# Optimization experiments

Measured on AMD Instinct MI355X. Metric: run time of the kernel, lower is better.

The kernel has to match this reference:

```python
import jax, jax.numpy as jnp
import numpy as np

HEADS = 8
DIM_HEAD = 64
WINDOW = 8  # local_window_size


def _sn_weight(W, u, sigma):
    """SNLinear reparameterized weight: one power-iteration step (detached)
    then sigma_W = v^T W u (grad flows through W only), weight = W/sigma_W * sigma."""
    v = W @ u
    v = v / jnp.linalg.norm(v)
    u2 = W.T @ v
    u2 = u2 / jnp.linalg.norm(u2)
    v = jax.lax.stop_gradient(v)
    u2 = jax.lax.stop_gradient(u2)
    sigma_w = jnp.einsum('c,cd,d->', v, W, u2)
    return W / sigma_w * sigma


def setup_inputs() -> dict:
    key = jax.random.key(0)
    ks = jax.random.split(key, 6)
    B, S, D = 2, 2048, 512
    inner = HEADS * DIM_HEAD  # 512
    x = jax.random.normal(ks[0], (B, S, D), dtype=jnp.float32)
    W_qkv = 0.02 * jax.random.normal(ks[1], (3 * inner, D), dtype=jnp.float32)
    u_qkv = jax.random.normal(ks[2], (D,), dtype=jnp.float32)
    u_qkv = u_qkv / jnp.linalg.norm(u_qkv)
    W_out = 0.02 * jax.random.normal(ks[3], (D, inner), dtype=jnp.float32)
    b_out = jnp.zeros((D,), dtype=jnp.float32)
    u_out = jax.random.normal(ks[4], (inner,), dtype=jnp.float32)
    u_out = u_out / jnp.linalg.norm(u_out)
    sigma_qkv = jnp.ones((1,), dtype=jnp.float32)
    sigma_out = jnp.ones((1,), dtype=jnp.float32)
    temperature = jnp.asarray(np.log(DIM_HEAD ** -0.5), dtype=jnp.float32)
    return {
        'x': x, 'W_qkv': W_qkv, 'u_qkv': u_qkv, 'sigma_qkv': sigma_qkv,
        'W_out': W_out, 'b_out': b_out, 'u_out': u_out, 'sigma_out': sigma_out,
        'temperature': temperature,
    }


def reference(x, W_qkv, u_qkv, sigma_qkv, W_out, b_out, u_out, sigma_out, temperature):
    B, S, D = x.shape
    # qkv projection (spectral-normed, no bias)
    Wq = _sn_weight(W_qkv, u_qkv, sigma_qkv[0])
    qkv = x @ Wq.T                                   # [B,S,3*inner]
    q, k, v = jnp.split(qkv, 3, axis=-1)
    to_heads = lambda t: t.reshape(B, S, HEADS, DIM_HEAD).transpose(0, 2, 1, 3)
    q, k, v = to_heads(q), to_heads(k), to_heads(v)   # [B,H,S,Dh]
    dots = jnp.einsum('bhid,bhjd->bhij', q, k) * jnp.exp(temperature)
    # local causal band mask (True inside band); original masked_fill fills True
    i = jnp.arange(S)
    band = (i[:, None] >= i[None, :]) & ((i[:, None] - i[None, :]) <= (WINDOW - 1))
    neg = -jnp.finfo(dots.dtype).max
    dots = jnp.where(band[None, None, :, :], neg, dots)
    attn = jax.nn.softmax(dots, axis=-1)
    out = jnp.einsum('bhij,bhjd->bhid', attn, v)      # [B,H,S,Dh]
    out = out.transpose(0, 2, 1, 3).reshape(B, S, HEADS * DIM_HEAD)
    Wo = _sn_weight(W_out, u_out, sigma_out[0])
    return out @ Wo.T + b_out
```

## Files before the change

### kernel.cpp

```cpp
#include <hip/hip_runtime.h>
#include <hip/hip_bf16.h>
#include <math.h>

#define HEADS 8
#define DH 64
#define SEQ 2048
#define BATCH 2
#define DMODEL 512
#define INNER 512
#define WIN 8

typedef unsigned short ushort_t;
typedef __attribute__((ext_vector_type(8))) __bf16 bf16x8;
typedef __attribute__((ext_vector_type(8))) unsigned short u16x8;
typedef __attribute__((ext_vector_type(4))) float f32x4;

__device__ inline float bf2f(ushort_t u) {
    unsigned v = ((unsigned)u) << 16; float f; __builtin_memcpy(&f, &v, 4); return f;
}
__device__ inline ushort_t f2bf(float f) {
    __hip_bfloat16 h = __float2bfloat16(f); ushort_t u; __builtin_memcpy(&u, &h, 2); return u;
}
__device__ inline int swz_idx(int row, int col) { return ((row << 6) | col) ^ ((row & 7) << 3); }

__device__ inline bf16x8 ld_frag(const ushort_t* lds, int row, int col) {
    u16x8 v = *(const u16x8*)&lds[swz_idx(row, col)];
    return __builtin_bit_cast(bf16x8, v);
}
__device__ inline f32x4 mfma16(bf16x8 a, bf16x8 b, f32x4 c) {
    return __builtin_amdgcn_mfma_f32_16x16x32_bf16(a, b, c, 0, 0, 0);
}
__device__ inline void gload16(const void* g, void* l) {
    __builtin_amdgcn_global_load_lds(
        (const __attribute__((address_space(1))) unsigned int*)g,
        (__attribute__((address_space(3))) unsigned int*)l, 16, 0, 0);
}

__global__ __launch_bounds__(256) void fused_cast_sn1(const float* __restrict__ x,
                                                      const float* __restrict__ Wq,
                                                      const float* __restrict__ Wo,
                                                      const float* __restrict__ uq,
                                                      const float* __restrict__ uo,
                                                      ushort_t* __restrict__ xb,
                                                      ushort_t* __restrict__ wqb,
                                                      ushort_t* __restrict__ wob,
                                                      float* __restrict__ zbuf,
                                                      float* __restrict__ v1,
                                                      float* __restrict__ v2) {
    const int b = blockIdx.x;
    if (b < 1536) {
        const int gid = b * 256 + threadIdx.x;
        const float* src; ushort_t* dst; int g;
        if (gid < 262144)      { src = x;  dst = xb;  g = gid; }
        else if (gid < 360448) { src = Wq; dst = wqb; g = gid - 262144; }
        else                   { src = Wo; dst = wob; g = gid - 360448; }
        float4 a = *(const float4*)&src[(size_t)g * 8];
        float4 c = *(const float4*)&src[(size_t)g * 8 + 4];
        u16x8 o;
        o[0] = f2bf(a.x); o[1] = f2bf(a.y); o[2] = f2bf(a.z); o[3] = f2bf(a.w);
        o[4] = f2bf(c.x); o[5] = f2bf(c.y); o[6] = f2bf(c.z); o[7] = f2bf(c.w);
        *(u16x8*)&dst[(size_t)g * 8] = o;
        if (gid < 1032) zbuf[gid] = 0.f;
    } else {
        const int lane = threadIdx.x & 63, w = threadIdx.x >> 6;
        const int r = (b - 1536) * 4 + w;
        const float* W; const float* u; float* vout; int rr;
        if (r < 1536) { W = Wq; u = uq; vout = v1; rr = r; }
        else          { W = Wo; u = uo; vout = v2; rr = r - 1536; }
        float4 w0 = *(const float4*)&W[(size_t)rr * 512 + lane * 8];
        float4 w1 = *(const float4*)&W[(size_t)rr * 512 + lane * 8 + 4];
        float4 u0 = *(const float4*)&u[lane * 8];
        float4 u1 = *(const float4*)&u[lane * 8 + 4];
        float dot = w0.x * u0.x + w0.y * u0.y + w0.z * u0.z + w0.w * u0.w +
                    w1.x * u1.x + w1.y * u1.y + w1.z * u1.z + w1.w * u1.w;
#pragma unroll
        for (int off = 1; off < 64; off <<= 1) dot += __shfl_xor(dot, off, 64);
        if (lane == 0) vout[rr] = dot;
    }
}

__global__ __launch_bounds__(256) void fused_sn2_sn3(const float* __restrict__ Wq,
                                                     const float* __restrict__ Wo,
                                                     const float* __restrict__ v1,
                                                     const float* __restrict__ v2,
                                                     float* __restrict__ z1,
                                                     float* __restrict__ z2,
                                                     float* __restrict__ counter,
                                                     const float* __restrict__ sq,
                                                     const float* __restrict__ so,
                                                     float* __restrict__ scales) {
    __shared__ float red[256];
    __shared__ int is_last;
    const int t = threadIdx.x, b = blockIdx.x;
    {
        const float* W; const float* v; float* z; int r0;
        if (b < 96) { W = Wq; v = v1; z = z1; r0 = b * 16; }
        else        { W = Wo; v = v2; z = z2; r0 = (b - 96) * 16; }
        float a0 = 0.f, a1 = 0.f;
        for (int i = 0; i < 16; ++i) {
            float vv = v[r0 + i];
            a0 += W[(size_t)(r0 + i) * 512 + t] * vv;
            a1 += W[(size_t)(r0 + i) * 512 + 256 + t] * vv;
        }
        atomicAdd(&z[t], a0);
        atomicAdd(&z[t + 256], a1);
    }
    __threadfence();
    __syncthreads();
    if (t == 0) is_last = (atomicAdd(counter, 1.0f) == 127.0f);
    __syncthreads();
    if (!is_last) return;
    __threadfence();
    for (int which = 0; which < 2; ++which) {
        const float* v = which ? v2 : v1;
        const float* z = which ? z2 : z1;
        const int R = which ? 512 : 1536;
        float n1 = 0.f;
        for (int i = t; i < R; i += 256) { float q = v[i]; n1 += q * q; }
        red[t] = n1; __syncthreads();
        for (int off = 128; off > 0; off >>= 1) { if (t < off) red[t] += red[t + off]; __syncthreads(); }
        n1 = red[0]; __syncthreads();
        float n2 = 0.f;
        for (int i = t; i < 512; i += 256) { float q = z[i]; n2 += q * q; }
        red[t] = n2; __syncthreads();
        for (int off = 128; off > 0; off >>= 1) { if (t < off) red[t] += red[t + off]; __syncthreads(); }
        if (t == 0) scales[which] = (which ? so[0] : sq[0]) * sqrtf(n1 / red[0]);
        __syncthreads();
    }
}

__global__ __launch_bounds__(256) void gemm_bt_qkv(const ushort_t* __restrict__ A,
                                                   const ushort_t* __restrict__ B,
                                                   ushort_t* __restrict__ qkv) {
    constexpr int K = DMODEL;
    __shared__ ushort_t As[8 * 128 * 8];
    __shared__ ushort_t Bs[8 * 128 * 8];
    const int t = threadIdx.x, lane = t & 63, w = t >> 6;
    const int wm = w >> 1, wn = w & 1, lg = lane >> 4, li = lane & 15;
    const int m0 = blockIdx.y * 128, n0 = blockIdx.x * 128;
    f32x4 acc[4][4] = {};
    for (int k0 = 0; k0 < K; k0 += 64) {
        __syncthreads();
#pragma unroll
        for (int i = 0; i < 4; ++i) {
            int j = w * 4 + i;
            int kc = j >> 1, mh = (j & 1) * 64;
            gload16(&A[(size_t)(m0 + mh + lane) * K + k0 + kc * 8], &As[(kc * 128 + mh) * 8]);
            gload16(&B[(size_t)(n0 + mh + lane) * K + k0 + kc * 8], &Bs[(kc * 128 + mh) * 8]);
        }
        __syncthreads();
#pragma unroll
        for (int kw = 0; kw < 2; ++kw) {
            bf16x8 af[4], bf[4];
#pragma unroll
            for (int mi = 0; mi < 4; ++mi)
                af[mi] = *(const bf16x8*)&As[((kw * 4 + lg) * 128 + wm * 64 + mi * 16 + li) * 8];
#pragma unroll
            for (int ni = 0; ni < 4; ++ni)
                bf[ni] = *(const bf16x8*)&Bs[((kw * 4 + lg) * 128 + wn * 64 + ni * 16 + li) * 8];
#pragma unroll
            for (int mi = 0; mi < 4; ++mi)
#pragma unroll
                for (int ni = 0; ni < 4; ++ni)
                    acc[mi][ni] = mfma16(af[mi], bf[ni], acc[mi][ni]);
        }
    }
    ushort_t* vT = qkv + (size_t)2 * BATCH * HEADS * SEQ * DH;
    if (n0 >= 1024) {
#pragma unroll
        for (int mi = 0; mi < 4; ++mi) {
            int base = m0 + wm * 64 + mi * 16 + lg * 4;
            int bb = base >> 11, ss = base & 2047;
#pragma unroll
            for (int ni = 0; ni < 4; ++ni) {
                int n = n0 + wn * 64 + ni * 16 + li;
                int h = (n >> 6) & 7, d0 = n & 63;
                ushort4 o;
                o.x = f2bf(acc[mi][ni][0]); o.y = f2bf(acc[mi][ni][1]);
                o.z = f2bf(acc[mi][ni][2]); o.w = f2bf(acc[mi][ni][3]);
                *(ushort4*)&vT[((size_t)((bb * HEADS + h) * DH) + d0) * SEQ + ss] = o;
            }
        }
    } else {
#pragma unroll
        for (int mi = 0; mi < 4; ++mi)
#pragma unroll
            for (int r = 0; r < 4; ++r) {
                int row = m0 + wm * 64 + mi * 16 + lg * 4 + r;
                int bb = row >> 11, ss = row & 2047;
#pragma unroll
                for (int ni = 0; ni < 4; ++ni) {
                    int n = n0 + wn * 64 + ni * 16 + li;
                    int which = n >> 9, h = (n >> 6) & 7, d0 = n & 63;
                    qkv[(size_t)which * (BATCH * HEADS * SEQ * DH) +
                        ((size_t)((bb * HEADS + h) * SEQ) + ss) * DH + d0] = f2bf(acc[mi][ni][r]);
                }
            }
    }
}

__global__ __launch_bounds__(256) void gemm_bt_out(const ushort_t* __restrict__ A,
                                                   const ushort_t* __restrict__ B,
                                                   const float* __restrict__ scales,
                                                   const float* __restrict__ bias,
                                                   float* __restrict__ C) {
    constexpr int K = INNER;
    __shared__ ushort_t As[8 * 128 * 8];
    __shared__ ushort_t Bs[8 * 128 * 8];
    const int t = threadIdx.x, lane = t & 63, w = t >> 6;
    const int wm = w >> 1, wn = w & 1, lg = lane >> 4, li = lane & 15;
    const int m0 = blockIdx.y * 128, n0 = blockIdx.x * 128;
    f32x4 acc[4][4] = {};
    for (int k0 = 0; k0 < K; k0 += 64) {
        __syncthreads();
#pragma unroll
        for (int i = 0; i < 4; ++i) {
            int j = w * 4 + i;
            int kc = j >> 1, mh = (j & 1) * 64;
            gload16(&A[(size_t)(m0 + mh + lane) * K + k0 + kc * 8], &As[(kc * 128 + mh) * 8]);
            gload16(&B[(size_t)(n0 + mh + lane) * K + k0 + kc * 8], &Bs[(kc * 128 + mh) * 8]);
        }
        __syncthreads();
#pragma unroll
        for (int kw = 0; kw < 2; ++kw) {
            bf16x8 af[4], bf[4];
#pragma unroll
            for (int mi = 0; mi < 4; ++mi)
                af[mi] = *(const bf16x8*)&As[((kw * 4 + lg) * 128 + wm * 64 + mi * 16 + li) * 8];
#pragma unroll
            for (int ni = 0; ni < 4; ++ni)
                bf[ni] = *(const bf16x8*)&Bs[((kw * 4 + lg) * 128 + wn * 64 + ni * 16 + li) * 8];
#pragma unroll
            for (int mi = 0; mi < 4; ++mi)
#pragma unroll
                for (int ni = 0; ni < 4; ++ni)
                    acc[mi][ni] = mfma16(af[mi], bf[ni], acc[mi][ni]);
        }
    }
    const float sc = scales[0] * scales[1];
#pragma unroll
    for (int mi = 0; mi < 4; ++mi)
#pragma unroll
        for (int r = 0; r < 4; ++r) {
            int row = m0 + wm * 64 + mi * 16 + lg * 4 + r;
#pragma unroll
            for (int ni = 0; ni < 4; ++ni) {
                int n = n0 + wn * 64 + ni * 16 + li;
                C[(size_t)row * INNER + n] = acc[mi][ni][r] * sc + bias[n];
            }
        }
}

__global__ __launch_bounds__(512) void attn_mfma_kernel(const ushort_t* __restrict__ qkv,
                                                        const float* __restrict__ temp,
                                                        const float* __restrict__ scales,
                                                        ushort_t* __restrict__ attn_out) {
    __shared__ ushort_t kvbuf[2 * 4 * 4096];
    __shared__ ushort_t Pl[2 * 4096];
    const int t    = threadIdx.x;
    const int lane = t & 63, w = t >> 6;
    const int g    = w >> 2, wl = w & 3;
    const int lg   = lane >> 4, li = lane & 15;
    const int bh   = blockIdx.x >> 5;
    const int i0   = (blockIdx.x & 31) * 64;
    const ushort_t* qp  = qkv;
    const ushort_t* kp  = qkv + (size_t)BATCH * HEADS * SEQ * DH;
    const ushort_t* vTp = kp  + (size_t)BATCH * HEADS * SEQ * DH;
    const float s0 = scales[0];
    const float st = expf(temp[0]) * s0 * s0;

    const int srow = t >> 3, sch = (t & 7) * 8;
    const ushort_t* kbase = kp  + (size_t)bh * SEQ * DH + (size_t)srow * DH + sch;
    const ushort_t* vbase = vTp + (size_t)bh * DH * SEQ + (size_t)srow * SEQ + sch;
    const int sdst = swz_idx(srow, sch);
    ushort_t* Pb = Pl + g * 4096;

    bf16x8 aQ[2];
#pragma unroll
    for (int c = 0; c < 2; ++c) {
        u16x8 qv = *(const u16x8*)&qp[((size_t)bh * SEQ + i0 + 16 * wl + li) * DH + 32 * c + lg * 8];
        u16x8 r;
#pragma unroll
        for (int j = 0; j < 8; ++j) r[j] = f2bf(bf2f(qv[j]) * st);
        aQ[c] = __builtin_bit_cast(bf16x8, r);
    }

    float lsum[4] = {0.f, 0.f, 0.f, 0.f};
    f32x4 oacc[4] = {};
    u16x8 pre0, pre1, pre2, pre3;

    pre0 = *(const u16x8*)(kbase);
    pre1 = *(const u16x8*)(kbase + (size_t)64 * DH);
    pre2 = *(const u16x8*)(vbase);
    pre3 = *(const u16x8*)(vbase + 64);
    {
        ushort_t* bfr = kvbuf;
        *(u16x8*)&bfr[sdst]         = pre0;
        *(u16x8*)&bfr[4096 + sdst]  = pre1;
        *(u16x8*)&bfr[8192 + sdst]  = pre2;
        *(u16x8*)&bfr[12288 + sdst] = pre3;
    }
    __syncthreads();

    int cur = 0;
    for (int jt = 0; jt < SEQ / 128; ++jt) {
        if (jt < SEQ / 128 - 1) {
            const size_t ko = (size_t)(jt + 1) * 128 * DH;
            const size_t vo = (size_t)(jt + 1) * 128;
            pre0 = *(const u16x8*)(kbase + ko);
            pre1 = *(const u16x8*)(kbase + ko + (size_t)64 * DH);
            pre2 = *(const u16x8*)(vbase + vo);
            pre3 = *(const u16x8*)(vbase + vo + 64);
        }
        const ushort_t* Kb = kvbuf + cur * 16384 + g * 4096;
        const ushort_t* Vb = kvbuf + cur * 16384 + 8192 + g * 4096;
        const int j0 = jt * 128 + g * 64;

        f32x4 s[4];
#pragma unroll
        for (int kc = 0; kc < 4; ++kc) {
            bf16x8 b0 = ld_frag(Kb, kc * 16 + li, lg * 8);
            bf16x8 b1 = ld_frag(Kb, kc * 16 + li, 32 + lg * 8);
            f32x4 z = {0.f, 0.f, 0.f, 0.f};
            z = mfma16(aQ[0], b0, z);
            z = mfma16(aQ[1], b1, z);
            s[kc] = z;
        }
        const bool need_mask = (j0 == i0) || (j0 == i0 - 64);
        if (need_mask) {
#pragma unroll
            for (int kc = 0; kc < 4; ++kc)
#pragma unroll
                for (int r = 0; r < 4; ++r) {
                    int qi = i0 + 16 * wl + lg * 4 + r;
                    int kj = j0 + kc * 16 + li;
                    float pv = ((unsigned)(qi - kj) < (unsigned)WIN) ? 0.f : __expf(s[kc][r]);
                    lsum[r] += pv;
                    Pb[swz_idx(16 * wl + lg * 4 + r, kc * 16 + li)] = f2bf(pv);
                }
        } else {
#pragma unroll
            for (int kc = 0; kc < 4; ++kc)
#pragma unroll
                for (int r = 0; r < 4; ++r) {
                    float pv = __expf(s[kc][r]);
                    lsum[r] += pv;
                    Pb[swz_idx(16 * wl + lg * 4 + r, kc * 16 + li)] = f2bf(pv);
                }
        }
        bf16x8 aP[2];
#pragma unroll
        for (int c = 0; c < 2; ++c) aP[c] = ld_frag(Pb, 16 * wl + li, c * 32 + lg * 8);
#pragma unroll
        for (int tt = 0; tt < 4; ++tt) {
            bf16x8 b0 = ld_frag(Vb, tt * 16 + li, lg * 8);
            bf16x8 b1 = ld_frag(Vb, tt * 16 + li, 32 + lg * 8);
            oacc[tt] = mfma16(aP[0], b0, oacc[tt]);
            oacc[tt] = mfma16(aP[1], b1, oacc[tt]);
        }
        if (jt < SEQ / 128 - 1) {
            ushort_t* bfr = kvbuf + (cur ^ 1) * 16384;
            *(u16x8*)&bfr[sdst]         = pre0;
            *(u16x8*)&bfr[4096 + sdst]  = pre1;
            *(u16x8*)&bfr[8192 + sdst]  = pre2;
            *(u16x8*)&bfr[12288 + sdst] = pre3;
        }
        __syncthreads();
        cur ^= 1;
    }

#pragma unroll
    for (int r = 0; r < 4; ++r) {
        float l = lsum[r];
        l += __shfl_xor(l, 1, 16);
        l += __shfl_xor(l, 2, 16);
        l += __shfl_xor(l, 4, 16);
        l += __shfl_xor(l, 8, 16);
        lsum[r] = l;
    }
    float* O_part = (float*)kvbuf;
    float* lsr    = (float*)Pl;
    if (g == 1) {
#pragma unroll
        for (int r = 0; r < 4; ++r) {
            int row = 16 * wl + lg * 4 + r;
            if (li == 0) lsr[row] = lsum[r];
#pragma unroll
            for (int tt = 0; tt < 4; ++tt)
                O_part[row * 68 + tt * 16 + li] = oacc[tt][r];
        }
    }
    __syncthreads();
    if (g == 0) {
        const int b_ = bh >> 3, h = bh & 7;
#pragma unroll
        for (int r = 0; r < 4; ++r) {
            int row = 16 * wl + lg * 4 + r;
            float inv = 1.0f / (lsum[r] + lsr[row]);
            size_t base = ((size_t)(b_ * SEQ + i0 + row)) * INNER + h * DH;
#pragma unroll
            for (int tt = 0; tt < 4; ++tt)
                attn_out[base + tt * 16 + li] =
                    f2bf((oacc[tt][r] + O_part[row * 68 + tt * 16 + li]) * inv);
        }
    }
}

extern "C" void kernel_launch(void* const* d_in, const int* in_sizes, int n_in,
                              void* d_out, int out_size, void* d_ws, size_t ws_size,
                              hipStream_t stream) {
    const float* x     = (const float*)d_in[0];
    const float* W_qkv = (const float*)d_in[1];
    const float* u_qkv = (const float*)d_in[2];
    const float* s_qkv = (const float*)d_in[3];
    const float* W_out = (const float*)d_in[4];
    const float* b_out = (const float*)d_in[5];
    const float* u_out = (const float*)d_in[6];
    const float* s_out = (const float*)d_in[7];
    const float* temp  = (const float*)d_in[8];
    float* out = (float*)d_out;

    float* scales  = (float*)d_ws;
    float* v1      = scales + 64;
    float* v2      = v1 + 1536;
    float* z1      = v2 + 512;
    float* z2      = z1 + 512;
    float* counter = z1 + 1024;
    ushort_t* xb    = (ushort_t*)((char*)d_ws + 16384);
    ushort_t* wqb   = xb + (size_t)2097152;
    ushort_t* wob   = wqb + (size_t)786432;
    ushort_t* qkvb  = wob + (size_t)262144;
    ushort_t* attnb = qkvb + (size_t)6291456;

    fused_cast_sn1<<<dim3(2048), dim3(256), 0, stream>>>(x, W_qkv, W_out, u_qkv, u_out,
                                                         xb, wqb, wob, z1, v1, v2);
    fused_sn2_sn3<<<dim3(128), dim3(256), 0, stream>>>(W_qkv, W_out, v1, v2, z1, z2,
                                                       counter, s_qkv, s_out, scales);
    gemm_bt_qkv<<<dim3(12, 32), dim3(256), 0, stream>>>(xb, wqb, qkvb);
    attn_mfma_kernel<<<dim3(512), dim3(512), 0, stream>>>(qkvb, temp, scales, attnb);
    gemm_bt_out<<<dim3(4, 32), dim3(256), 0, stream>>>(attnb, wob, scales, b_out, out);
}
```

Before: 166.2 us.

## Shrink GEMM tiles, async LDS staging in attention, exp2 and wave priority

The QKV GEMM moves to 128x64 tiles and the output GEMM to 64x64 tiles, which launches more workgroups and spreads work across more CUs. The attention kernel swaps its register-prefetch-then-LDS-store staging of K/V for direct global-to-LDS async loads issued ahead of compute. It also folds log2(e) into the scale so it can use the hardware exp2, and raises wave priority around the MFMA sections. The smaller GEMM tiles trade register reuse for occupancy and give less data reuse per tile. The async loads depend on the new pre-swizzled address mapping being correct.

```diff
diff --git a/kernel.cpp b/kernel.cpp
--- a/kernel.cpp
+++ b/kernel.cpp
@@ -21,6 +21,7 @@
 __device__ inline ushort_t f2bf(float f) {
     __hip_bfloat16 h = __float2bfloat16(f); ushort_t u; __builtin_memcpy(&u, &h, 2); return u;
 }
+__device__ inline float fast_exp2(float x) { return __builtin_amdgcn_exp2f(x); }
 __device__ inline int swz_idx(int row, int col) { return ((row << 6) | col) ^ ((row & 7) << 3); }
 
 __device__ inline bf16x8 ld_frag(const ushort_t* lds, int row, int col) {
@@ -134,11 +135,11 @@
                                                    ushort_t* __restrict__ qkv) {
     constexpr int K = DMODEL;
     __shared__ ushort_t As[8 * 128 * 8];
-    __shared__ ushort_t Bs[8 * 128 * 8];
+    __shared__ ushort_t Bs[8 * 64 * 8];
     const int t = threadIdx.x, lane = t & 63, w = t >> 6;
     const int wm = w >> 1, wn = w & 1, lg = lane >> 4, li = lane & 15;
-    const int m0 = blockIdx.y * 128, n0 = blockIdx.x * 128;
-    f32x4 acc[4][4] = {};
+    const int m0 = blockIdx.y * 128, n0 = blockIdx.x * 64;
+    f32x4 acc[4][2] = {};
     for (int k0 = 0; k0 < K; k0 += 64) {
         __syncthreads();
 #pragma unroll
@@ -146,22 +147,26 @@
             int j = w * 4 + i;
             int kc = j >> 1, mh = (j & 1) * 64;
             gload16(&A[(size_t)(m0 + mh + lane) * K + k0 + kc * 8], &As[(kc * 128 + mh) * 8]);
-            gload16(&B[(size_t)(n0 + mh + lane) * K + k0 + kc * 8], &Bs[(kc * 128 + mh) * 8]);
+        }
+#pragma unroll
+        for (int i = 0; i < 2; ++i) {
+            int kc = w * 2 + i;
+            gload16(&B[(size_t)(n0 + lane) * K + k0 + kc * 8], &Bs[(kc * 64) * 8]);
         }
         __syncthreads();
 #pragma unroll
         for (int kw = 0; kw < 2; ++kw) {
-            bf16x8 af[4], bf[4];
+            bf16x8 af[4], bf[2];
 #pragma unroll
             for (int mi = 0; mi < 4; ++mi)
                 af[mi] = *(const bf16x8*)&As[((kw * 4 + lg) * 128 + wm * 64 + mi * 16 + li) * 8];
 #pragma unroll
-            for (int ni = 0; ni < 4; ++ni)
-                bf[ni] = *(const bf16x8*)&Bs[((kw * 4 + lg) * 128 + wn * 64 + ni * 16 + li) * 8];
+            for (int ni = 0; ni < 2; ++ni)
+                bf[ni] = *(const bf16x8*)&Bs[((kw * 4 + lg) * 64 + wn * 32 + ni * 16 + li) * 8];
 #pragma unroll
             for (int mi = 0; mi < 4; ++mi)
 #pragma unroll
-                for (int ni = 0; ni < 4; ++ni)
+                for (int ni = 0; ni < 2; ++ni)
                     acc[mi][ni] = mfma16(af[mi], bf[ni], acc[mi][ni]);
         }
     }
@@ -172,8 +177,8 @@
             int base = m0 + wm * 64 + mi * 16 + lg * 4;
             int bb = base >> 11, ss = base & 2047;
 #pragma unroll
-            for (int ni = 0; ni < 4; ++ni) {
-                int n = n0 + wn * 64 + ni * 16 + li;
+            for (int ni = 0; ni < 2; ++ni) {
+                int n = n0 + wn * 32 + ni * 16 + li;
                 int h = (n >> 6) & 7, d0 = n & 63;
                 ushort4 o;
                 o.x = f2bf(acc[mi][ni][0]); o.y = f2bf(acc[mi][ni][1]);
@@ -189,8 +194,8 @@
                 int row = m0 + wm * 64 + mi * 16 + lg * 4 + r;
                 int bb = row >> 11, ss = row & 2047;
 #pragma unroll
-                for (int ni = 0; ni < 4; ++ni) {
-                    int n = n0 + wn * 64 + ni * 16 + li;
+                for (int ni = 0; ni < 2; ++ni) {
+                    int n = n0 + wn * 32 + ni * 16 + li;
                     int which = n >> 9, h = (n >> 6) & 7, d0 = n & 63;
                     qkv[(size_t)which * (BATCH * HEADS * SEQ * DH) +
                         ((size_t)((bb * HEADS + h) * SEQ) + ss) * DH + d0] = f2bf(acc[mi][ni][r]);
@@ -205,47 +210,46 @@
                                                    const float* __restrict__ bias,
                                                    float* __restrict__ C) {
     constexpr int K = INNER;
-    __shared__ ushort_t As[8 * 128 * 8];
-    __shared__ ushort_t Bs[8 * 128 * 8];
+    __shared__ ushort_t As[8 * 64 * 8];
+    __shared__ ushort_t Bs[8 * 64 * 8];
     const int t = threadIdx.x, lane = t & 63, w = t >> 6;
     const int wm = w >> 1, wn = w & 1, lg = lane >> 4, li = lane & 15;
-    const int m0 = blockIdx.y * 128, n0 = blockIdx.x * 128;
-    f32x4 acc[4][4] = {};
+    const int m0 = blockIdx.y * 64, n0 = blockIdx.x * 64;
+    f32x4 acc[2][2] = {};
     for (int k0 = 0; k0 < K; k0 += 64) {
         __syncthreads();
 #pragma unroll
-        for (int i = 0; i < 4; ++i) {
-            int j = w * 4 + i;
-            int kc = j >> 1, mh = (j & 1) * 64;
-            gload16(&A[(size_t)(m0 + mh + lane) * K + k0 + kc * 8], &As[(kc * 128 + mh) * 8]);
-            gload16(&B[(size_t)(n0 + mh + lane) * K + k0 + kc * 8], &Bs[(kc * 128 + mh) * 8]);
+        for (int i = 0; i < 2; ++i) {
+            int kc = w * 2 + i;
+            gload16(&A[(size_t)(m0 + lane) * K + k0 + kc * 8], &As[(kc * 64) * 8]);
+            gload16(&B[(size_t)(n0 + lane) * K + k0 + kc * 8], &Bs[(kc * 64) * 8]);
         }
         __syncthreads();
 #pragma unroll
         for (int kw = 0; kw < 2; ++kw) {
-            bf16x8 af[4], bf[4];
-#pragma unroll
-            for (int mi = 0; mi < 4; ++mi)
-                af[mi] = *(const bf16x8*)&As[((kw * 4 + lg) * 128 + wm * 64 + mi * 16 + li) * 8];
-#pragma unroll
-            for (int ni = 0; ni < 4; ++ni)
-                bf[ni] = *(const bf16x8*)&Bs[((kw * 4 + lg) * 128 + wn * 64 + ni * 16 + li) * 8];
-#pragma unroll
-            for (int mi = 0; mi < 4; ++mi)
-#pragma unroll
-                for (int ni = 0; ni < 4; ++ni)
+            bf16x8 af[2], bf[2];
+#pragma unroll
+            for (int mi = 0; mi < 2; ++mi)
+                af[mi] = *(const bf16x8*)&As[((kw * 4 + lg) * 64 + wm * 32 + mi * 16 + li) * 8];
+#pragma unroll
+            for (int ni = 0; ni < 2; ++ni)
+                bf[ni] = *(const bf16x8*)&Bs[((kw * 4 + lg) * 64 + wn * 32 + ni * 16 + li) * 8];
+#pragma unroll
+            for (int mi = 0; mi < 2; ++mi)
+#pragma unroll
+                for (int ni = 0; ni < 2; ++ni)
                     acc[mi][ni] = mfma16(af[mi], bf[ni], acc[mi][ni]);
         }
     }
     const float sc = scales[0] * scales[1];
 #pragma unroll
-    for (int mi = 0; mi < 4; ++mi)
+    for (int mi = 0; mi < 2; ++mi)
 #pragma unroll
         for (int r = 0; r < 4; ++r) {
-            int row = m0 + wm * 64 + mi * 16 + lg * 4 + r;
-#pragma unroll
-            for (int ni = 0; ni < 4; ++ni) {
-                int n = n0 + wn * 64 + ni * 16 + li;
+            int row = m0 + wm * 32 + mi * 16 + lg * 4 + r;
+#pragma unroll
+            for (int ni = 0; ni < 2; ++ni) {
+                int n = n0 + wn * 32 + ni * 16 + li;
                 C[(size_t)row * INNER + n] = acc[mi][ni][r] * sc + bias[n];
             }
         }
@@ -266,14 +270,14 @@
     const ushort_t* qp  = qkv;
     const ushort_t* kp  = qkv + (size_t)BATCH * HEADS * SEQ * DH;
     const ushort_t* vTp = kp  + (size_t)BATCH * HEADS * SEQ * DH;
+    const ushort_t* kp_bh  = kp  + (size_t)bh * SEQ * DH;
+    const ushort_t* vTp_bh = vTp + (size_t)bh * DH * SEQ;
     const float s0 = scales[0];
-    const float st = expf(temp[0]) * s0 * s0;
-
-    const int srow = t >> 3, sch = (t & 7) * 8;
-    const ushort_t* kbase = kp  + (size_t)bh * SEQ * DH + (size_t)srow * DH + sch;
-    const ushort_t* vbase = vTp + (size_t)bh * DH * SEQ + (size_t)srow * SEQ + sch;
-    const int sdst = swz_idx(srow, sch);
+    const float st = expf(temp[0]) * s0 * s0 * 1.44269504088896340736f;
+
     ushort_t* Pb = Pl + g * 4096;
+    const int srw = lane >> 3;
+    const int sc  = (lane & 7) ^ srw;
 
     bf16x8 aQ[2];
 #pragma unroll
@@ -287,36 +291,35 @@
 
     float lsum[4] = {0.f, 0.f, 0.f, 0.f};
     f32x4 oacc[4] = {};
-    u16x8 pre0, pre1, pre2, pre3;
-
-    pre0 = *(const u16x8*)(kbase);
-    pre1 = *(const u16x8*)(kbase + (size_t)64 * DH);
-    pre2 = *(const u16x8*)(vbase);
-    pre3 = *(const u16x8*)(vbase + 64);
-    {
-        ushort_t* bfr = kvbuf;
-        *(u16x8*)&bfr[sdst]         = pre0;
-        *(u16x8*)&bfr[4096 + sdst]  = pre1;
-        *(u16x8*)&bfr[8192 + sdst]  = pre2;
-        *(u16x8*)&bfr[12288 + sdst] = pre3;
-    }
+
+    auto STAGE = [&](int jtn, int tbuf) {
+#pragma unroll
+        for (int i = 0; i < 4; ++i) {
+            const int sid = i * 8 + w;
+            const int bsel = sid >> 3;
+            const int srow8 = sid & 7;
+            const int row = srow8 * 8 + srw;
+            const ushort_t* gsrc;
+            if (bsel < 2)
+                gsrc = kp_bh + (size_t)(jtn * 128 + bsel * 64 + row) * DH + sc * 8;
+            else
+                gsrc = vTp_bh + (size_t)row * SEQ + jtn * 128 + (bsel - 2) * 64 + sc * 8;
+            gload16(gsrc, &kvbuf[tbuf * 16384 + bsel * 4096 + srow8 * 512]);
+        }
+    };
+
+    STAGE(0, 0);
     __syncthreads();
 
     int cur = 0;
     for (int jt = 0; jt < SEQ / 128; ++jt) {
-        if (jt < SEQ / 128 - 1) {
-            const size_t ko = (size_t)(jt + 1) * 128 * DH;
-            const size_t vo = (size_t)(jt + 1) * 128;
-            pre0 = *(const u16x8*)(kbase + ko);
-            pre1 = *(const u16x8*)(kbase + ko + (size_t)64 * DH);
-            pre2 = *(const u16x8*)(vbase + vo);
-            pre3 = *(const u16x8*)(vbase + vo + 64);
-        }
+        if (jt < SEQ / 128 - 1) STAGE(jt + 1, cur ^ 1);
         const ushort_t* Kb = kvbuf + cur * 16384 + g * 4096;
         const ushort_t* Vb = kvbuf + cur * 16384 + 8192 + g * 4096;
         const int j0 = jt * 128 + g * 64;
 
         f32x4 s[4];
+        __builtin_amdgcn_s_setprio(1);
 #pragma unroll
         for (int kc = 0; kc < 4; ++kc) {
             bf16x8 b0 = ld_frag(Kb, kc * 16 + li, lg * 8);
@@ -326,6 +329,7 @@
             z = mfma16(aQ[1], b1, z);
             s[kc] = z;
         }
+        __builtin_amdgcn_s_setprio(0);
         const bool need_mask = (j0 == i0) || (j0 == i0 - 64);
         if (need_mask) {
 #pragma unroll
@@ -334,7 +338,7 @@
                 for (int r = 0; r < 4; ++r) {
                     int qi = i0 + 16 * wl + lg * 4 + r;
                     int kj = j0 + kc * 16 + li;
-                    float pv = ((unsigned)(qi - kj) < (unsigned)WIN) ? 0.f : __expf(s[kc][r]);
+                    float pv = ((unsigned)(qi - kj) < (unsigned)WIN) ? 0.f : fast_exp2(s[kc][r]);
                     lsum[r] += pv;
                     Pb[swz_idx(16 * wl + lg * 4 + r, kc * 16 + li)] = f2bf(pv);
                 }
@@ -343,7 +347,7 @@
             for (int kc = 0; kc < 4; ++kc)
 #pragma unroll
                 for (int r = 0; r < 4; ++r) {
-                    float pv = __expf(s[kc][r]);
+                    float pv = fast_exp2(s[kc][r]);
                     lsum[r] += pv;
                     Pb[swz_idx(16 * wl + lg * 4 + r, kc * 16 + li)] = f2bf(pv);
                 }
@@ -351,6 +355,7 @@
         bf16x8 aP[2];
 #pragma unroll
         for (int c = 0; c < 2; ++c) aP[c] = ld_frag(Pb, 16 * wl + li, c * 32 + lg * 8);
+        __builtin_amdgcn_s_setprio(1);
 #pragma unroll
         for (int tt = 0; tt < 4; ++tt) {
             bf16x8 b0 = ld_frag(Vb, tt * 16 + li, lg * 8);
@@ -358,13 +363,7 @@
             oacc[tt] = mfma16(aP[0], b0, oacc[tt]);
             oacc[tt] = mfma16(aP[1], b1, oacc[tt]);
         }
-        if (jt < SEQ / 128 - 1) {
-            ushort_t* bfr = kvbuf + (cur ^ 1) * 16384;
-            *(u16x8*)&bfr[sdst]         = pre0;
-            *(u16x8*)&bfr[4096 + sdst]  = pre1;
-            *(u16x8*)&bfr[8192 + sdst]  = pre2;
-            *(u16x8*)&bfr[12288 + sdst] = pre3;
-        }
+        __builtin_amdgcn_s_setprio(0);
         __syncthreads();
         cur ^= 1;
     }
@@ -436,7 +435,7 @@
                                                          xb, wqb, wob, z1, v1, v2);
     fused_sn2_sn3<<<dim3(128), dim3(256), 0, stream>>>(W_qkv, W_out, v1, v2, z1, z2,
                                                        counter, s_qkv, s_out, scales);
-    gemm_bt_qkv<<<dim3(12, 32), dim3(256), 0, stream>>>(xb, wqb, qkvb);
+    gemm_bt_qkv<<<dim3(24, 32), dim3(256), 0, stream>>>(xb, wqb, qkvb);
     attn_mfma_kernel<<<dim3(512), dim3(512), 0, stream>>>(qkvb, temp, scales, attnb);
-    gemm_bt_out<<<dim3(4, 32), dim3(256), 0, stream>>>(attnb, wob, scales, b_out, out);
-}
+    gemm_bt_out<<<dim3(8, 64), dim3(256), 0, stream>>>(attnb, wob, scales, b_out, out);
+}
```

New measurement: 160.9 us. 3.2% less time.
